# Optimization experiments

Measured on AMD Instinct MI355X. Metric: run time of the kernel, lower is better.

The kernel has to match this reference:

```python
import jax, jax.numpy as jnp
import numpy as np

N_NODES = 100000
N_EDGES = 1600000
D_IN = 128
D_HID = 128
N_CLS = 2


def gcn_conv(x, edge_index, W, b):
    """PyG GCNConv: add self-loops, symmetric normalization, linear, scatter-add, bias."""
    n = x.shape[0]
    loop = jnp.arange(n, dtype=edge_index.dtype)
    src = jnp.concatenate([edge_index[0], loop])  # [E+N]
    dst = jnp.concatenate([edge_index[1], loop])
    # degree computed on destination (col) after adding self-loops
    deg = jax.ops.segment_sum(jnp.ones_like(dst, dtype=x.dtype), dst, num_segments=n)
    dinv = jnp.where(deg > 0, jax.lax.rsqrt(deg), 0.0)
    norm = dinv[src] * dinv[dst]  # [E+N]
    h = x @ W  # [N, out]
    msg = h[src] * norm[:, None]  # [E+N, out]
    out = jax.ops.segment_sum(msg, dst, num_segments=n)
    return out + b


def setup_inputs() -> dict:
    key = jax.random.key(0)
    k1, k2, k3, k4 = jax.random.split(key, 4)
    x = jax.random.normal(k1, (N_NODES, D_IN), dtype=jnp.float32)
    edge_index = jax.random.randint(k2, (2, N_EDGES), 0, N_NODES, dtype=jnp.int64)
    W1 = jax.random.normal(k3, (D_IN, D_HID), dtype=jnp.float32) * (1.0 / np.sqrt(D_IN))
    b1 = jnp.zeros((D_HID,), dtype=jnp.float32)
    W2 = jax.random.normal(k4, (D_HID, N_CLS), dtype=jnp.float32) * (1.0 / np.sqrt(D_HID))
    b2 = jnp.zeros((N_CLS,), dtype=jnp.float32)
    return {"x": x, "edge_index": edge_index, "W1": W1, "b1": b1, "W2": W2, "b2": b2}


def reference(x, edge_index, W1, b1, W2, b2):
    h = gcn_conv(x, edge_index, W1, b1)
    h = jax.nn.relu(h)
    # training=False -> dropout skipped
    out = gcn_conv(h, edge_index, W2, b2)
    return out
```

## Files before the change

### kernel.cpp

```cpp
#include <hip/hip_runtime.h>
#include <hip/hip_fp16.h>
#include <cstdint>
#include <cstddef>

#define NN 100000
#define NE 1600000
#define D 128
#define NBK 782
#define NBLK_P 512
#define EPB 3125

typedef _Float16 half8 __attribute__((ext_vector_type(8)));
typedef _Float16 half4v __attribute__((ext_vector_type(4)));
typedef float f32x4 __attribute__((ext_vector_type(4)));


__launch_bounds__(256)
__global__ void p1_count_k(const int* __restrict__ ei, unsigned* __restrict__ offs) {
    __shared__ unsigned hist[NBK];
    int tid = threadIdx.x, b = blockIdx.x;
    for (int k = tid; k < NBK; k += 256) hist[k] = 0u;
    __syncthreads();
    int e0 = b * EPB;
    for (int i = tid; i < EPB; i += 256) {
        int d = ei[NE + e0 + i];
        atomicAdd(&hist[d >> 7], 1u);
    }
    __syncthreads();
    for (int k = tid; k < NBK; k += 256) offs[(size_t)b * NBK + k] = hist[k];
}

__launch_bounds__(512)
__global__ void p2a_k(unsigned* __restrict__ offs, unsigned* __restrict__ base) {
    __shared__ unsigned sh[512];
    int t = threadIdx.x, k = blockIdx.x;
    unsigned v = offs[(size_t)t * NBK + k];
    sh[t] = v;
    __syncthreads();
    for (int off = 1; off < 512; off <<= 1) {
        unsigned u = (t >= off) ? sh[t - off] : 0u;
        __syncthreads();
        sh[t] += u;
        __syncthreads();
    }
    offs[(size_t)t * NBK + k] = sh[t] - v;
    if (t == 511) base[k] = sh[511];
}

__global__ void p2b_k(unsigned* __restrict__ base) {
    __shared__ unsigned sh[1024];
    int t = threadIdx.x;
    unsigned v = (t < NBK) ? base[t] : 0u;
    sh[t] = v;
    __syncthreads();
    for (int off = 1; off < 1024; off <<= 1) {
        unsigned u = (t >= off) ? sh[t - off] : 0u;
        __syncthreads();
        sh[t] += u;
        __syncthreads();
    }
    if (t < NBK) base[t] = sh[t] - v;
    if (t == NBK) base[NBK] = sh[NBK - 1];
}

__launch_bounds__(256)
__global__ void p3_scatter_k(const int* __restrict__ ei, const unsigned* __restrict__ offs,
                             const unsigned* __restrict__ base, unsigned* __restrict__ part) {
    __shared__ unsigned lcnt[NBK];
    int tid = threadIdx.x, b = blockIdx.x;
    for (int k = tid; k < NBK; k += 256) lcnt[k] = base[k] + offs[(size_t)b * NBK + k];
    __syncthreads();
    int e0 = b * EPB;
    for (int i = tid; i < EPB; i += 256) {
        int s = ei[e0 + i];
        int d = ei[NE + e0 + i];
        unsigned pos = atomicAdd(&lcnt[d >> 7], 1u);
        part[pos] = (unsigned)s | ((unsigned)(d & 127) << 20);
    }
}

__launch_bounds__(256)
__global__ void p4_csr_k(const unsigned* __restrict__ part, const unsigned* __restrict__ base,
                         unsigned* __restrict__ rp, float* __restrict__ dinv,
                         unsigned* __restrict__ col) {
    __shared__ unsigned c[128], p[128], run[128];
    int tid = threadIdx.x, k = blockIdx.x;
    int n0 = k << 7;
    int nodes = (NN - n0 < 128) ? (NN - n0) : 128;
    unsigned e0 = base[k], e1 = base[k + 1];

    if (tid < 128) c[tid] = 0u;
    __syncthreads();
    for (unsigned e = e0 + tid; e < e1; e += 256)
        atomicAdd(&c[(part[e] >> 20) & 127], 1u);
    __syncthreads();

    unsigned myc = (tid < 128) ? c[tid] : 0u;
    if (tid < 128) p[tid] = myc;
    __syncthreads();
    for (int off = 1; off < 128; off <<= 1) {
        unsigned u = 0;
        if (tid < 128 && tid >= off) u = p[tid - off];
        __syncthreads();
        if (tid < 128) p[tid] += u;
        __syncthreads();
    }
    if (tid < 128) {
        unsigned excl = p[tid] - myc;
        run[tid] = excl;
        if (tid < nodes) {
            rp[n0 + tid] = e0 + excl;
            dinv[n0 + tid] = rsqrtf((float)(myc + 1u));
        }
    }
    if (k == 0 && tid == 0) rp[NN] = NE;
    __syncthreads();

    for (unsigned e = e0 + tid; e < e1; e += 256) {
        unsigned v = part[e];
        unsigned dlo = (v >> 20) & 127;
        unsigned pos = e0 + atomicAdd(&run[dlo], 1u);
        col[pos] = v & 0xFFFFFu;
    }
}

__global__ void wt_k(const float* __restrict__ W, _Float16* __restrict__ Wt) {
    int idx = blockIdx.x * 256 + threadIdx.x;
    int n = idx >> 7, k = idx & 127;
    Wt[idx] = (_Float16)W[k * 128 + n];
}

__launch_bounds__(256)
__global__ void gemm1_k(const float* __restrict__ x, const _Float16* __restrict__ Wt,
                        const float* __restrict__ dinv, _Float16* __restrict__ h) {
    __shared__ _Float16 xs[64 * 136];
    int tid = threadIdx.x;
    int rb = blockIdx.x * 64;
    int w = tid >> 6, lane = tid & 63;
    int m = lane & 15, q4 = lane >> 4;

#pragma unroll
    for (int q = 0; q < 8; q++) {
        int idx = q * 256 + tid;
        int row = idx >> 5;
        int c4 = (idx & 31) * 4;
        int gr = rb + row;
        float4 v = (gr < NN) ? *(const float4*)(x + (size_t)gr * 128 + c4)
                             : make_float4(0, 0, 0, 0);
        half4v hv = { (_Float16)v.x, (_Float16)v.y, (_Float16)v.z, (_Float16)v.w };
        *(half4v*)(&xs[row * 136 + c4]) = hv;
    }
    __syncthreads();

    f32x4 acc[8];
#pragma unroll
    for (int nt = 0; nt < 8; nt++) acc[nt] = (f32x4){0.f, 0.f, 0.f, 0.f};

    const _Float16* arow = &xs[(w * 16 + m) * 136 + q4 * 8];
    const _Float16* brow = Wt + m * 128 + q4 * 8;
#pragma unroll
    for (int kc = 0; kc < 4; kc++) {
        half8 af = *(const half8*)(arow + kc * 32);
#pragma unroll
        for (int nt = 0; nt < 8; nt++) {
            half8 bf = *(const half8*)(brow + nt * 16 * 128 + kc * 32);
            acc[nt] = __builtin_amdgcn_mfma_f32_16x16x32_f16(af, bf, acc[nt], 0, 0, 0);
        }
    }

    float dv[4];
#pragma unroll
    for (int r = 0; r < 4; r++) {
        int ri = rb + w * 16 + q4 * 4 + r;
        dv[r] = (ri < NN) ? dinv[ri] : 0.f;
    }
    __syncthreads();
#pragma unroll
    for (int nt = 0; nt < 8; nt++) {
#pragma unroll
        for (int r = 0; r < 4; r++) {
            xs[(w * 16 + q4 * 4 + r) * 136 + nt * 16 + m] = (_Float16)(acc[nt][r] * dv[r]);
        }
    }
    __syncthreads();
#pragma unroll
    for (int q = 0; q < 4; q++) {
        int idx = q * 256 + tid;
        int row = idx >> 4;
        int c8 = (idx & 15) * 8;
        int gr = rb + row;
        if (gr < NN)
            *(half8*)(h + (size_t)gr * 128 + c8) = *(const half8*)(&xs[row * 136 + c8]);
    }
}

#define GATHER(sv, vv) \
    { unsigned s_ = __builtin_amdgcn_readfirstlane(col[sv]); \
      vv = __half22float2(hb[(size_t)(s_ * 64u + lane)]); }

__launch_bounds__(256)
__global__ void agg1_k(const _Float16* __restrict__ h, const unsigned* __restrict__ rp,
                       const unsigned* __restrict__ col, const float* __restrict__ dinv,
                       const float* __restrict__ b1, const float* __restrict__ W2,
                       float* __restrict__ z) {
    int i = (blockIdx.x * 256 + threadIdx.x) >> 6;
    int lane = threadIdx.x & 63;
    if (i >= NN) return;

    const __half2* hb = (const __half2*)h;
    float di = dinv[i];
    float2 hv = __half22float2(hb[(size_t)i * 64 + lane]);
    float ax = hv.x, ay = hv.y;

    unsigned p0 = __builtin_amdgcn_readfirstlane(rp[i]);
    unsigned p1 = __builtin_amdgcn_readfirstlane(rp[i + 1]);
    unsigned e = p0;
    for (; e + 16 <= p1; e += 16) {
        float2 v0, v1, v2, v3, v4, v5, v6, v7, v8, v9, va, vb, vc, vd, ve, vf;
        GATHER(e, v0)      GATHER(e + 1, v1)  GATHER(e + 2, v2)  GATHER(e + 3, v3)
        GATHER(e + 4, v4)  GATHER(e + 5, v5)  GATHER(e + 6, v6)  GATHER(e + 7, v7)
        GATHER(e + 8, v8)  GATHER(e + 9, v9)  GATHER(e + 10, va) GATHER(e + 11, vb)
        GATHER(e + 12, vc) GATHER(e + 13, vd) GATHER(e + 14, ve) GATHER(e + 15, vf)
        ax += ((v0.x + v1.x) + (v2.x + v3.x)) + ((v4.x + v5.x) + (v6.x + v7.x))
            + ((v8.x + v9.x) + (va.x + vb.x)) + ((vc.x + vd.x) + (ve.x + vf.x));
        ay += ((v0.y + v1.y) + (v2.y + v3.y)) + ((v4.y + v5.y) + (v6.y + v7.y))
            + ((v8.y + v9.y) + (va.y + vb.y)) + ((vc.y + vd.y) + (ve.y + vf.y));
    }
    for (; e + 4 <= p1; e += 4) {
        float2 v0, v1, v2, v3;
        GATHER(e, v0) GATHER(e + 1, v1) GATHER(e + 2, v2) GATHER(e + 3, v3)
        ax += (v0.x + v1.x) + (v2.x + v3.x);
        ay += (v0.y + v1.y) + (v2.y + v3.y);
    }
    for (; e < p1; ++e) {
        float2 v;
        GATHER(e, v)
        ax += v.x;
        ay += v.y;
    }
    ax *= di;
    ay *= di;

    float2 bv = ((const float2*)b1)[lane];
    float h0 = fmaxf(ax + bv.x, 0.f);
    float h1 = fmaxf(ay + bv.y, 0.f);

    float4 w = ((const float4*)W2)[lane];
    float pz0 = fmaf(h0, w.x, h1 * w.z);
    float pz1 = fmaf(h0, w.y, h1 * w.w);
#pragma unroll
    for (int off = 32; off > 0; off >>= 1) {
        pz0 += __shfl_down(pz0, off);
        pz1 += __shfl_down(pz1, off);
    }
    if (lane == 0) {
        float2* zp = (float2*)(z + (size_t)i * 2);
        *zp = make_float2(pz0 * di, pz1 * di);
    }
}

__launch_bounds__(256)
__global__ void agg2_k(const float* __restrict__ z, const unsigned* __restrict__ rp,
                       const unsigned* __restrict__ col, const float* __restrict__ dinv,
                       const float* __restrict__ b2, float* __restrict__ out) {
    int i = (blockIdx.x * 256 + threadIdx.x) >> 6;
    int lane = threadIdx.x & 63;
    if (i >= NN) return;

    float di = dinv[i];
    unsigned p0 = __builtin_amdgcn_readfirstlane(rp[i]);
    unsigned p1 = __builtin_amdgcn_readfirstlane(rp[i + 1]);
    float a0 = 0.f, a1 = 0.f;
    for (unsigned e = p0 + lane; e < p1; e += 64) {
        unsigned s = col[e];
        float2 v = ((const float2*)z)[s];
        a0 += v.x;
        a1 += v.y;
    }
#pragma unroll
    for (int off = 32; off > 0; off >>= 1) {
        a0 += __shfl_down(a0, off);
        a1 += __shfl_down(a1, off);
    }
    if (lane == 0) {
        float2 zi = ((const float2*)z)[i];
        out[(size_t)i * 2]     = (a0 + zi.x) * di + b2[0];
        out[(size_t)i * 2 + 1] = (a1 + zi.y) * di + b2[1];
    }
}

extern "C" void kernel_launch(void* const* d_in, const int* in_sizes, int n_in,
                              void* d_out, int out_size, void* d_ws, size_t ws_size,
                              hipStream_t stream) {
    const float* x  = (const float*)d_in[0];
    const int*   ei = (const int*)d_in[1];
    const float* W1 = (const float*)d_in[2];
    const float* b1 = (const float*)d_in[3];
    const float* W2 = (const float*)d_in[4];
    const float* b2 = (const float*)d_in[5];
    float* out = (float*)d_out;

    char* ws = (char*)d_ws;
    unsigned* part = (unsigned*)(ws);
    unsigned* offs = (unsigned*)(ws + 6400000);
    unsigned* base = (unsigned*)(ws + 8100000);
    _Float16* h    = (_Float16*)(ws);
    float*    z    = (float*)(ws + 25600000);
    float*    dinv = (float*)(ws + 26400000);
    unsigned* rp   = (unsigned*)(ws + 26800000);
    unsigned* col  = (unsigned*)(ws + 27200016);
    _Float16* Wt   = (_Float16*)(ws + 33600016);

    wt_k<<<64, 256, 0, stream>>>(W1, Wt);
    p1_count_k<<<NBLK_P, 256, 0, stream>>>(ei, offs);
    p2a_k<<<NBK, 512, 0, stream>>>(offs, base);
    p2b_k<<<1, 1024, 0, stream>>>(base);
    p3_scatter_k<<<NBLK_P, 256, 0, stream>>>(ei, offs, base, part);
    p4_csr_k<<<NBK, 256, 0, stream>>>(part, base, rp, dinv, col);

    gemm1_k<<<(NN + 63) / 64, 256, 0, stream>>>(x, Wt, dinv, h);
    agg1_k<<<(NN + 3) / 4, 256, 0, stream>>>(h, rp, col, dinv, b1, W2, z);
    agg2_k<<<(NN + 3) / 4, 256, 0, stream>>>(z, rp, col, dinv, b2, out);
}
```

Before: 262.7 us.

## Shrink partition block count, stage W1 in LDS, use 16-lane groups in agg2

Three separate changes. Histogram/scatter partitioning now uses 200 blocks of 8000 edges instead of 512, which shrinks the offsets table and the per-bucket scan to 256 threads. gemm1 copies the transposed fp16 weight into padded shared memory so B fragments come from LDS rather than global loads. agg2 assigns 16 lanes per node instead of a full 64-lane wave, matching the average degree of about 16 to cut idle lanes. Fewer partition blocks reduce parallelism in the count and scatter phases, and the extra LDS in gemm1 may lower occupancy.

```diff
diff --git a/kernel.cpp b/kernel.cpp
--- a/kernel.cpp
+++ b/kernel.cpp
@@ -7,8 +7,8 @@
 #define NE 1600000
 #define D 128
 #define NBK 782
-#define NBLK_P 512
-#define EPB 3125
+#define NBLK_P 200
+#define EPB 8000
 
 typedef _Float16 half8 __attribute__((ext_vector_type(8)));
 typedef _Float16 half4v __attribute__((ext_vector_type(4)));
@@ -30,21 +30,21 @@
     for (int k = tid; k < NBK; k += 256) offs[(size_t)b * NBK + k] = hist[k];
 }
 
-__launch_bounds__(512)
+__launch_bounds__(256)
 __global__ void p2a_k(unsigned* __restrict__ offs, unsigned* __restrict__ base) {
-    __shared__ unsigned sh[512];
+    __shared__ unsigned sh[256];
     int t = threadIdx.x, k = blockIdx.x;
-    unsigned v = offs[(size_t)t * NBK + k];
+    unsigned v = (t < NBLK_P) ? offs[(size_t)t * NBK + k] : 0u;
     sh[t] = v;
     __syncthreads();
-    for (int off = 1; off < 512; off <<= 1) {
+    for (int off = 1; off < 256; off <<= 1) {
         unsigned u = (t >= off) ? sh[t - off] : 0u;
         __syncthreads();
         sh[t] += u;
         __syncthreads();
     }
-    offs[(size_t)t * NBK + k] = sh[t] - v;
-    if (t == 511) base[k] = sh[511];
+    if (t < NBLK_P) offs[(size_t)t * NBK + k] = sh[t] - v;
+    if (t == 255) base[k] = sh[255];
 }
 
 __global__ void p2b_k(unsigned* __restrict__ base) {
@@ -133,12 +133,20 @@
 __launch_bounds__(256)
 __global__ void gemm1_k(const float* __restrict__ x, const _Float16* __restrict__ Wt,
                         const float* __restrict__ dinv, _Float16* __restrict__ h) {
+    __shared__ _Float16 wt[128 * 136];
     __shared__ _Float16 xs[64 * 136];
     int tid = threadIdx.x;
     int rb = blockIdx.x * 64;
     int w = tid >> 6, lane = tid & 63;
     int m = lane & 15, q4 = lane >> 4;
 
+#pragma unroll
+    for (int q = 0; q < 8; q++) {
+        int idx = q * 256 + tid;
+        int n  = idx >> 4;
+        int k8 = (idx & 15) * 8;
+        *(half8*)(&wt[n * 136 + k8]) = *(const half8*)(Wt + n * 128 + k8);
+    }
 #pragma unroll
     for (int q = 0; q < 8; q++) {
         int idx = q * 256 + tid;
@@ -157,13 +165,12 @@
     for (int nt = 0; nt < 8; nt++) acc[nt] = (f32x4){0.f, 0.f, 0.f, 0.f};
 
     const _Float16* arow = &xs[(w * 16 + m) * 136 + q4 * 8];
-    const _Float16* brow = Wt + m * 128 + q4 * 8;
 #pragma unroll
     for (int kc = 0; kc < 4; kc++) {
         half8 af = *(const half8*)(arow + kc * 32);
 #pragma unroll
         for (int nt = 0; nt < 8; nt++) {
-            half8 bf = *(const half8*)(brow + nt * 16 * 128 + kc * 32);
+            half8 bf = *(const half8*)(&wt[(nt * 16 + m) * 136 + q4 * 8 + kc * 32]);
             acc[nt] = __builtin_amdgcn_mfma_f32_16x16x32_f16(af, bf, acc[nt], 0, 0, 0);
         }
     }
@@ -263,26 +270,25 @@
 __global__ void agg2_k(const float* __restrict__ z, const unsigned* __restrict__ rp,
                        const unsigned* __restrict__ col, const float* __restrict__ dinv,
                        const float* __restrict__ b2, float* __restrict__ out) {
-    int i = (blockIdx.x * 256 + threadIdx.x) >> 6;
-    int lane = threadIdx.x & 63;
+    int i = (blockIdx.x * 256 + threadIdx.x) >> 4;
+    int sl = threadIdx.x & 15;
     if (i >= NN) return;
 
-    float di = dinv[i];
-    unsigned p0 = __builtin_amdgcn_readfirstlane(rp[i]);
-    unsigned p1 = __builtin_amdgcn_readfirstlane(rp[i + 1]);
+    unsigned p0 = rp[i], p1 = rp[i + 1];
     float a0 = 0.f, a1 = 0.f;
-    for (unsigned e = p0 + lane; e < p1; e += 64) {
+    for (unsigned e = p0 + sl; e < p1; e += 16) {
         unsigned s = col[e];
         float2 v = ((const float2*)z)[s];
         a0 += v.x;
         a1 += v.y;
     }
 #pragma unroll
-    for (int off = 32; off > 0; off >>= 1) {
-        a0 += __shfl_down(a0, off);
-        a1 += __shfl_down(a1, off);
-    }
-    if (lane == 0) {
+    for (int off = 8; off > 0; off >>= 1) {
+        a0 += __shfl_down(a0, off, 16);
+        a1 += __shfl_down(a1, off, 16);
+    }
+    if (sl == 0) {
+        float di = dinv[i];
         float2 zi = ((const float2*)z)[i];
         out[(size_t)i * 2]     = (a0 + zi.x) * di + b2[0];
         out[(size_t)i * 2 + 1] = (a1 + zi.y) * di + b2[1];
@@ -303,7 +309,7 @@
     char* ws = (char*)d_ws;
     unsigned* part = (unsigned*)(ws);
     unsigned* offs = (unsigned*)(ws + 6400000);
-    unsigned* base = (unsigned*)(ws + 8100000);
+    unsigned* base = (unsigned*)(ws + 7100000);
     _Float16* h    = (_Float16*)(ws);
     float*    z    = (float*)(ws + 25600000);
     float*    dinv = (float*)(ws + 26400000);
@@ -313,12 +319,12 @@
 
     wt_k<<<64, 256, 0, stream>>>(W1, Wt);
     p1_count_k<<<NBLK_P, 256, 0, stream>>>(ei, offs);
-    p2a_k<<<NBK, 512, 0, stream>>>(offs, base);
+    p2a_k<<<NBK, 256, 0, stream>>>(offs, base);
     p2b_k<<<1, 1024, 0, stream>>>(base);
     p3_scatter_k<<<NBLK_P, 256, 0, stream>>>(ei, offs, base, part);
     p4_csr_k<<<NBK, 256, 0, stream>>>(part, base, rp, dinv, col);
 
     gemm1_k<<<(NN + 63) / 64, 256, 0, stream>>>(x, Wt, dinv, h);
     agg1_k<<<(NN + 3) / 4, 256, 0, stream>>>(h, rp, col, dinv, b1, W2, z);
-    agg2_k<<<(NN + 3) / 4, 256, 0, stream>>>(z, rp, col, dinv, b2, out);
-}
+    agg2_k<<<(NN * 16 + 255) / 256, 256, 0, stream>>>(z, rp, col, dinv, b2, out);
+}
```

Measured after the change: 228.4 us. 1.15x faster.
